# Kernel optimization log

Hardware: AMD Instinct MI355X
Metric: run time of the kernel (lower is better)

The kernel has to match this reference:

```python
import jax, jax.numpy as jnp
import numpy as np

HEADS = 16
GRID_SIZE = 5      # efficient-KAN default
SPLINE_ORDER = 3   # efficient-KAN default


def _grid(in_features, dtype):
    # grid_range = [-1, 1]
    h = 2.0 / GRID_SIZE
    g = jnp.arange(-SPLINE_ORDER, GRID_SIZE + SPLINE_ORDER + 1, dtype=dtype) * h - 1.0
    return jnp.broadcast_to(g, (in_features, g.shape[0]))  # (in, G)


def _b_splines(x, grid):
    # x: (N, in), grid: (in, G); Cox-de Boor recursion
    xg = x[:, :, None]
    bases = ((xg >= grid[:, :-1]) & (xg < grid[:, 1:])).astype(x.dtype)
    for k in range(1, SPLINE_ORDER + 1):
        bases = ((xg - grid[:, :-(k + 1)]) / (grid[:, k:-1] - grid[:, :-(k + 1)]) * bases[:, :, :-1]
                 + (grid[:, k + 1:] - xg) / (grid[:, k + 1:] - grid[:, 1:-k]) * bases[:, :, 1:])
    return bases  # (N, in, GRID_SIZE + SPLINE_ORDER)


def _kan_linear(x, base_w, spline_w, spline_scaler):
    grid = _grid(x.shape[-1], x.dtype)
    base = jax.nn.silu(x) @ base_w.T                      # (N, out)
    b = _b_splines(x, grid)                               # (N, in, K)
    sw = spline_w * spline_scaler[..., None]              # (out, in, K)
    return base + jnp.einsum('nik,oik->no', b, sw)


def setup_inputs():
    key = jax.random.key(0)
    S, H = 2048, 1024
    hd = H // HEADS
    K = GRID_SIZE + SPLINE_ORDER
    ks = jax.random.split(key, 6)
    x = jax.random.normal(ks[0], (S, H), jnp.float32)
    base_w = jax.random.normal(ks[1], (3 * H, H), jnp.float32) / np.float32(np.sqrt(H))
    spline_w = jax.random.normal(ks[2], (3 * H, H, K), jnp.float32) * 0.1
    spline_scaler = 1.0 + 0.1 * jax.random.normal(ks[3], (3 * H, H), jnp.float32)
    out_w = jax.random.normal(ks[4], (H, H), jnp.float32) / np.float32(np.sqrt(H))
    out_b = jnp.zeros((H,), jnp.float32)
    # RoPE rotation matrix (unit complex), theta = 10000
    t = jnp.arange(S, dtype=jnp.float32)
    freqs = 1.0 / (10000.0 ** (jnp.arange(0, hd, 2, dtype=jnp.float32) / hd))
    ang = jnp.outer(t, freqs)  # (S, hd//2)
    return {"x": x, "base_w": base_w, "spline_w": spline_w,
            "spline_scaler": spline_scaler, "out_w": out_w, "out_b": out_b,
            "rot_cos": jnp.cos(ang), "rot_sin": jnp.sin(ang)}


def reference(x, base_w, spline_w, spline_scaler, out_w, out_b, rot_cos, rot_sin):
    S, H = x.shape
    hd = H // HEADS
    qkv = _kan_linear(x, base_w, spline_w, spline_scaler)          # (S, 3H)
    qkv = qkv.reshape(1, S, HEADS, 3 * hd).transpose(0, 2, 1, 3)   # (1,h,S,3d)
    q, k, v = jnp.split(qkv, 3, axis=-1)                           # each (1,h,S,d)

    def rope(t):
        tp = t.reshape(1, HEADS, S, hd // 2, 2)
        c = rot_cos[None, None]
        s = rot_sin[None, None]
        re = tp[..., 0] * c - tp[..., 1] * s
        im = tp[..., 0] * s + tp[..., 1] * c
        return jnp.stack([re, im], axis=-1).reshape(1, HEADS, S, hd)

    q, k = rope(q), rope(k)
    scores = jnp.einsum('bhqd,bhkd->bhqk', q, k) / np.float32(np.sqrt(hd))
    attn = jax.nn.softmax(scores, axis=-1)
    ctx = jnp.einsum('bhqk,bhkd->bhqd', attn, v)
    ctx = ctx.transpose(0, 2, 1, 3).reshape(1, S, H)
    return ctx @ out_w.T + out_b
```

## Files before the change

### kernel.cpp

```cpp
#include <hip/hip_runtime.h>

typedef unsigned short u16;
typedef __bf16 bf16x8 __attribute__((ext_vector_type(8)));
typedef float f32x4 __attribute__((ext_vector_type(4)));

#define S_LEN 2048
#define NHEADS 16
#define HD 64
#define HDIM 1024
#define QKVN 3072
#define KAUG 9216

__device__ __forceinline__ u16 f2bf(float f) {
  union { float f; unsigned u; } v; v.f = f;
  unsigned r = v.u + 0x7fffu + ((v.u >> 16) & 1u);
  return (u16)(r >> 16);
}

typedef __attribute__((address_space(1))) const unsigned int gas_u32;
typedef __attribute__((address_space(3))) unsigned int las_u32;
__device__ __forceinline__ void gload_lds16(const void* g, void* l) {
  __builtin_amdgcn_global_load_lds((gas_u32*)g, (las_u32*)l, 16, 0, 0);
}

__global__ void prep_a_kernel(const float* __restrict__ x, u16* __restrict__ Aaug) {
  int idx = blockIdx.x * 256 + threadIdx.x;
  int n = idx >> 10, i = idx & 1023;
  float xv = x[idx];
  float sil = xv / (1.0f + __expf(-xv));
  Aaug[(size_t)n * KAUG + i] = f2bf(sil);

  float b[11];
#pragma unroll
  for (int j = 0; j < 11; ++j) {
    float t0 = 0.4f * (float)(j - 3) - 1.0f;
    float t1 = 0.4f * (float)(j - 2) - 1.0f;
    b[j] = (xv >= t0 && xv < t1) ? 1.0f : 0.0f;
  }
#pragma unroll
  for (int k = 1; k <= 3; ++k) {
    const float invk = (k == 1) ? 2.5f : (k == 2) ? 1.25f : 0.83333333f;
#pragma unroll
    for (int j = 0; j < 10; ++j) {
      if (j + k < 11) {
        float tj   = 0.4f * (float)(j - 3) - 1.0f;
        float tjk1 = 0.4f * (float)(j + k - 2) - 1.0f;
        b[j] = ((xv - tj) * b[j] + (tjk1 - xv) * b[j + 1]) * invk;
      }
    }
  }
  u16 t[8];
#pragma unroll
  for (int j = 0; j < 8; ++j) t[j] = f2bf(b[j]);
  uint4 pk;
  pk.x = (unsigned)t[0] | ((unsigned)t[1] << 16);
  pk.y = (unsigned)t[2] | ((unsigned)t[3] << 16);
  pk.z = (unsigned)t[4] | ((unsigned)t[5] << 16);
  pk.w = (unsigned)t[6] | ((unsigned)t[7] << 16);
  *reinterpret_cast<uint4*>(&Aaug[(size_t)n * KAUG + 1024 + i * 8]) = pk;
}

__global__ void prep_w_kernel(const float* __restrict__ bw, const float* __restrict__ sw,
                              const float* __restrict__ sc, u16* __restrict__ Waug) {
  int idx = blockIdx.x * 256 + threadIdx.x;
  int o = idx >> 10, i = idx & 1023;
  Waug[(size_t)o * KAUG + i] = f2bf(bw[idx]);
  float s = sc[idx];
  const float4* sp = reinterpret_cast<const float4*>(sw + (size_t)idx * 8);
  float4 a = sp[0], b = sp[1];
  uint4 pk;
  pk.x = (unsigned)f2bf(a.x * s) | ((unsigned)f2bf(a.y * s) << 16);
  pk.y = (unsigned)f2bf(a.z * s) | ((unsigned)f2bf(a.w * s) << 16);
  pk.z = (unsigned)f2bf(b.x * s) | ((unsigned)f2bf(b.y * s) << 16);
  pk.w = (unsigned)f2bf(b.z * s) | ((unsigned)f2bf(b.w * s) << 16);
  *reinterpret_cast<uint4*>(&Waug[(size_t)o * KAUG + 1024 + i * 8]) = pk;
}

__global__ void prep_ow_kernel(const float* __restrict__ ow, u16* __restrict__ owbf) {
  int idx = blockIdx.x * 256 + threadIdx.x;
  float4 v = reinterpret_cast<const float4*>(ow)[idx];
  uint2 pk;
  pk.x = (unsigned)f2bf(v.x) | ((unsigned)f2bf(v.y) << 16);
  pk.y = (unsigned)f2bf(v.z) | ((unsigned)f2bf(v.w) << 16);
  reinterpret_cast<uint2*>(owbf)[idx] = pk;
}

__global__ __launch_bounds__(256) void gemm_bt(
    const u16* __restrict__ A, const u16* __restrict__ B, float* __restrict__ C,
    int M, int N, int K, int Ksp)
{
  __shared__ u16 As[128 * 32];
  __shared__ u16 Bs[128 * 32];
  const int tid = threadIdx.x;
  const int lane = tid & 63;
  const int w = tid >> 6;
  const int wr = w >> 1, wc = w & 1;
  const int row0 = blockIdx.y * 128, col0 = blockIdx.x * 128;
  const int lr = lane & 15, lg = lane >> 4;
  const int kbeg = blockIdx.z * Ksp;
  const int nsteps = Ksp >> 5;
  float* Cz = C + (size_t)blockIdx.z * M * N;

  f32x4 acc[4][4];
#pragma unroll
  for (int m = 0; m < 4; ++m)
#pragma unroll
    for (int n = 0; n < 4; ++n) acc[m][n] = (f32x4){0.f, 0.f, 0.f, 0.f};

  const int arow = tid >> 2;
  const int kch  = tid & 3;
  const u16* ga = A + (size_t)(row0 + arow) * K + kbeg + kch * 8;
  const u16* gb = B + (size_t)(col0 + arow) * K + kbeg + kch * 8;
  const size_t rstep = (size_t)64 * K;

  for (int ks = 0; ks < nsteps; ++ks) {
    gload_lds16(ga, &As[tid * 8]);
    gload_lds16(ga + rstep, &As[2048 + tid * 8]);
    gload_lds16(gb, &Bs[tid * 8]);
    gload_lds16(gb + rstep, &Bs[2048 + tid * 8]);
    ga += 32; gb += 32;
    __syncthreads();

    bf16x8 af[4], bf[4];
#pragma unroll
    for (int m = 0; m < 4; ++m) {
      int r = wr * 64 + m * 16 + lr;
      af[m] = *reinterpret_cast<const bf16x8*>(&As[r * 32 + lg * 8]);
    }
#pragma unroll
    for (int n = 0; n < 4; ++n) {
      int r = wc * 64 + n * 16 + lr;
      bf[n] = *reinterpret_cast<const bf16x8*>(&Bs[r * 32 + lg * 8]);
    }
#pragma unroll
    for (int m = 0; m < 4; ++m)
#pragma unroll
      for (int n = 0; n < 4; ++n)
        acc[m][n] = __builtin_amdgcn_mfma_f32_16x16x32_bf16(af[m], bf[n], acc[m][n], 0, 0, 0);
    __syncthreads();
  }

#pragma unroll
  for (int m = 0; m < 4; ++m) {
    int row = row0 + wr * 64 + m * 16 + lg * 4;
#pragma unroll
    for (int n = 0; n < 4; ++n) {
      int col = col0 + wc * 64 + n * 16 + lr;
#pragma unroll
      for (int j = 0; j < 4; ++j)
        Cz[(size_t)(row + j) * N + col] = acc[m][n][j];
    }
  }
}

__global__ void reduce4_bias_kernel(const float* __restrict__ p, const float* __restrict__ bias,
                                    float* __restrict__ out) {
  int idx = blockIdx.x * 256 + threadIdx.x;
  const float4* p4 = reinterpret_cast<const float4*>(p);
  const size_t stride4 = (size_t)2048 * 1024 / 4;
  float4 a = p4[idx], b = p4[idx + stride4], c = p4[idx + 2 * stride4], d = p4[idx + 3 * stride4];
  float4 bv = reinterpret_cast<const float4*>(bias)[idx & 255];
  float4 r;
  r.x = a.x + b.x + c.x + d.x + bv.x;
  r.y = a.y + b.y + c.y + d.y + bv.y;
  r.z = a.z + b.z + c.z + d.z + bv.z;
  r.w = a.w + b.w + c.w + d.w + bv.w;
  reinterpret_cast<float4*>(out)[idx] = r;
}

__global__ void rope_kernel(const float* __restrict__ qkv0, const float* __restrict__ qkv1,
                            const float* __restrict__ rc, const float* __restrict__ rs,
                            u16* __restrict__ qro, u16* __restrict__ kro) {
  int idx = blockIdx.x * 256 + threadIdx.x;
  int h = idx >> 16;
  int rem = idx & 65535;
  int s = rem >> 5, i = rem & 31;
  size_t boff = (size_t)s * QKVN + h * 192 + 2 * i;
  float2 q0v = *reinterpret_cast<const float2*>(qkv0 + boff);
  float2 q1v = *reinterpret_cast<const float2*>(qkv1 + boff);
  float2 k0v = *reinterpret_cast<const float2*>(qkv0 + boff + 64);
  float2 k1v = *reinterpret_cast<const float2*>(qkv1 + boff + 64);
  float q0 = q0v.x + q1v.x, q1 = q0v.y + q1v.y;
  float k0 = k0v.x + k1v.x, k1 = k0v.y + k1v.y;
  float c = rc[s * 32 + i], sn = rs[s * 32 + i];
  size_t ob = ((size_t)(h * S_LEN + s)) * HD + 2 * i;
  unsigned qpk = (unsigned)f2bf((q0 * c - q1 * sn) * 0.125f) |
                 ((unsigned)f2bf((q0 * sn + q1 * c) * 0.125f) << 16);
  unsigned kpk = (unsigned)f2bf(k0 * c - k1 * sn) |
                 ((unsigned)f2bf(k0 * sn + k1 * c) << 16);
  *reinterpret_cast<unsigned*>(qro + ob) = qpk;
  *reinterpret_cast<unsigned*>(kro + ob) = kpk;
}

__global__ void vtrans_kernel(const float* __restrict__ qkv0, const float* __restrict__ qkv1,
                              u16* __restrict__ vT) {
  __shared__ float tile[64][65];
  int h = blockIdx.x >> 5;
  int st = blockIdx.x & 31;
  int s0 = st * 64;
  int t = threadIdx.x;
  int r = t >> 2, c4 = t & 3;
  size_t soff = (size_t)(s0 + r) * QKVN + h * 192 + 128 + c4 * 16;
  const float* src0 = qkv0 + soff;
  const float* src1 = qkv1 + soff;
#pragma unroll
  for (int z = 0; z < 4; ++z) {
    float4 v = *reinterpret_cast<const float4*>(src0 + z * 4);
    float4 u = *reinterpret_cast<const float4*>(src1 + z * 4);
    tile[r][c4 * 16 + z * 4 + 0] = v.x + u.x;
    tile[r][c4 * 16 + z * 4 + 1] = v.y + u.y;
    tile[r][c4 * 16 + z * 4 + 2] = v.z + u.z;
    tile[r][c4 * 16 + z * 4 + 3] = v.w + u.w;
  }
  __syncthreads();
  int d = t >> 2, sc = t & 3;
  u16* dst = vT + ((size_t)(h * 64 + d)) * S_LEN + s0 + sc * 16;
  unsigned wv[8];
#pragma unroll
  for (int z = 0; z < 8; ++z) {
    unsigned lo = f2bf(tile[sc * 16 + 2 * z][d]);
    unsigned hi = f2bf(tile[sc * 16 + 2 * z + 1][d]);
    wv[z] = lo | (hi << 16);
  }
  *reinterpret_cast<uint4*>(dst)     = make_uint4(wv[0], wv[1], wv[2], wv[3]);
  *reinterpret_cast<uint4*>(dst + 8) = make_uint4(wv[4], wv[5], wv[6], wv[7]);
}

__global__ __launch_bounds__(256) void attn_kernel(
    const u16* __restrict__ qro, const u16* __restrict__ kro,
    const u16* __restrict__ vT, u16* __restrict__ ctxb)
{
  const int lane = threadIdx.x & 63;
  const int w = threadIdx.x >> 6;
  const int bid = (blockIdx.x & 7) * 64 + (blockIdx.x >> 3);
  const int h = bid >> 5;
  const int qt = (bid & 31) * 4 + w;
  const int lr = lane & 15, lg = lane >> 4;

  const u16* qbase = qro + ((size_t)(h * S_LEN + qt * 16 + lr)) * HD + lg * 8;
  bf16x8 qa0 = *reinterpret_cast<const bf16x8*>(qbase);
  bf16x8 qa1 = *reinterpret_cast<const bf16x8*>(qbase + 32);

  float mrow = -3.0e38f, lrow = 0.f;
  f32x4 o[4];
#pragma unroll
  for (int n = 0; n < 4; ++n) o[n] = (f32x4){0.f, 0.f, 0.f, 0.f};

  const int sA = lr + 32 * (lg & 1);
  const int sB = sA + 16;
  const bool loHalf = (lg < 2);

  for (int kt = 0; kt < 64; ++kt) {
    const int key0 = kt * 32;
    const u16* kb = kro + ((size_t)(h * S_LEN + key0 + lr)) * HD + lg * 8;
    bf16x8 k00 = *reinterpret_cast<const bf16x8*>(kb);
    bf16x8 k01 = *reinterpret_cast<const bf16x8*>(kb + 32);
    bf16x8 k10 = *reinterpret_cast<const bf16x8*>(kb + (size_t)16 * HD);
    bf16x8 k11 = *reinterpret_cast<const bf16x8*>(kb + (size_t)16 * HD + 32);

    f32x4 s0 = (f32x4){0.f, 0.f, 0.f, 0.f};
    f32x4 s1 = (f32x4){0.f, 0.f, 0.f, 0.f};
    __builtin_amdgcn_s_setprio(1);
    s0 = __builtin_amdgcn_mfma_f32_16x16x32_bf16(k00, qa0, s0, 0, 0, 0);
    s0 = __builtin_amdgcn_mfma_f32_16x16x32_bf16(k01, qa1, s0, 0, 0, 0);
    s1 = __builtin_amdgcn_mfma_f32_16x16x32_bf16(k10, qa0, s1, 0, 0, 0);
    s1 = __builtin_amdgcn_mfma_f32_16x16x32_bf16(k11, qa1, s1, 0, 0, 0);
    __builtin_amdgcn_s_setprio(0);

    float vmax = fmaxf(fmaxf(fmaxf(s0[0], s0[1]), fmaxf(s0[2], s0[3])),
                       fmaxf(fmaxf(s1[0], s1[1]), fmaxf(s1[2], s1[3])));
    vmax = fmaxf(vmax, __shfl_xor(vmax, 16));
    vmax = fmaxf(vmax, __shfl_xor(vmax, 32));

    if (__any(vmax > mrow + 8.0f)) {
      float mnew = fmaxf(mrow, vmax);
      float al = __expf(mrow - mnew);
      float alO[4];
#pragma unroll
      for (int j = 0; j < 4; ++j) alO[j] = __shfl(al, lg * 4 + j);
#pragma unroll
      for (int n = 0; n < 4; ++n)
#pragma unroll
        for (int j = 0; j < 4; ++j) o[n][j] *= alO[j];
      lrow *= al;
      mrow = mnew;
    }

    float p[8];
#pragma unroll
    for (int j = 0; j < 4; ++j) {
      p[j]     = __expf(s0[j] - mrow);
      p[4 + j] = __expf(s1[j] - mrow);
    }
    lrow += ((p[0] + p[1]) + (p[2] + p[3])) + ((p[4] + p[5]) + (p[6] + p[7]));

    union { bf16x8 v; uint4 u; } pk_;
#pragma unroll
    for (int j = 0; j < 8; ++j) pk_.v[j] = (__bf16)p[j];

    unsigned a0 = __shfl((int)pk_.u.x, sA), a1 = __shfl((int)pk_.u.y, sA);
    unsigned a2 = __shfl((int)pk_.u.x, sB), a3 = __shfl((int)pk_.u.y, sB);
    unsigned b0 = __shfl((int)pk_.u.z, sA), b1 = __shfl((int)pk_.u.w, sA);
    unsigned b2 = __shfl((int)pk_.u.z, sB), b3 = __shfl((int)pk_.u.w, sB);
    union { uint4 u; bf16x8 v; } pa_;
    pa_.u.x = loHalf ? a0 : b0;
    pa_.u.y = loHalf ? a1 : b1;
    pa_.u.z = loHalf ? a2 : b2;
    pa_.u.w = loHalf ? a3 : b3;

    const u16* vb = vT + ((size_t)(h * 64 + lr)) * S_LEN + key0 + lg * 8;
    __builtin_amdgcn_s_setprio(1);
#pragma unroll
    for (int n = 0; n < 4; ++n) {
      bf16x8 vf = *reinterpret_cast<const bf16x8*>(vb + (size_t)(n * 16) * S_LEN);
      o[n] = __builtin_amdgcn_mfma_f32_16x16x32_bf16(pa_.v, vf, o[n], 0, 0, 0);
    }
    __builtin_amdgcn_s_setprio(0);
  }

  lrow += __shfl_xor(lrow, 16);
  lrow += __shfl_xor(lrow, 32);
  float linv[4];
#pragma unroll
  for (int j = 0; j < 4; ++j) linv[j] = 1.0f / __shfl(lrow, lg * 4 + j);

#pragma unroll
  for (int n = 0; n < 4; ++n) {
    int col = h * 64 + n * 16 + lr;
#pragma unroll
    for (int j = 0; j < 4; ++j) {
      int row = qt * 16 + lg * 4 + j;
      ctxb[(size_t)row * HDIM + col] = f2bf(o[n][j] * linv[j]);
    }
  }
}

extern "C" void kernel_launch(void* const* d_in, const int* in_sizes, int n_in,
                              void* d_out, int out_size, void* d_ws, size_t ws_size,
                              hipStream_t stream) {
  const float* x   = (const float*)d_in[0];
  const float* bw  = (const float*)d_in[1];
  const float* sw  = (const float*)d_in[2];
  const float* ssc = (const float*)d_in[3];
  const float* ow  = (const float*)d_in[4];
  const float* ob  = (const float*)d_in[5];
  const float* rc  = (const float*)d_in[6];
  const float* rs  = (const float*)d_in[7];
  float* out = (float*)d_out;

  char* ws = (char*)d_ws;
  u16*   Aaug  = (u16*)(ws);
  u16*   Waug  = (u16*)(ws + 37748736);
  float* qkv0  = (float*)(ws + 94371840);
  float* qkv1  = (float*)(ws + 119537664);
  u16*   qro   = (u16*)(ws + 144703488);
  u16*   kro   = (u16*)(ws + 148897792);
  u16*   vT    = (u16*)(ws + 153092096);
  u16*   owbf  = (u16*)(ws + 157286400);
  u16*   ctxb  = (u16*)(ws + 94371840);
  float* part  = (float*)(ws + 119537664);

  prep_a_kernel<<<8192, 256, 0, stream>>>(x, Aaug);
  prep_w_kernel<<<12288, 256, 0, stream>>>(bw, sw, ssc, Waug);
  prep_ow_kernel<<<1024, 256, 0, stream>>>(ow, owbf);

  gemm_bt<<<dim3(24, 16, 2), 256, 0, stream>>>(Aaug, Waug, qkv0, 2048, 3072, 9216, 4608);

  rope_kernel<<<4096, 256, 0, stream>>>(qkv0, qkv1, rc, rs, qro, kro);
  vtrans_kernel<<<512, 256, 0, stream>>>(qkv0, qkv1, vT);

  attn_kernel<<<512, 256, 0, stream>>>(qro, kro, vT, ctxb);

  gemm_bt<<<dim3(8, 16, 4), 256, 0, stream>>>(ctxb, owbf, part, 2048, 1024, 1024, 256);
  reduce4_bias_kernel<<<2048, 256, 0, stream>>>(part, ob, out);
}
```

Before: 499.5 us.

## Raise QKV GEMM split-K to four and prefetch K/V tiles in attention

The QKV GEMM split-K factor becomes four when the workspace is large enough, giving 768 blocks instead of 384 for better CU occupancy. The rope and vtrans kernels are generalised to sum a variable number of partial buffers. The attention loop now loads the next K tile one iteration ahead and issues the V loads early to hide memory latency. The cost is extra partial-buffer traffic and more registers in attention.

```diff
diff --git a/kernel.cpp b/kernel.cpp
--- a/kernel.cpp
+++ b/kernel.cpp
@@ -168,7 +168,7 @@
   reinterpret_cast<float4*>(out)[idx] = r;
 }
 
-__global__ void rope_kernel(const float* __restrict__ qkv0, const float* __restrict__ qkv1,
+__global__ void rope_kernel(const float* __restrict__ qkv, int nsplit,
                             const float* __restrict__ rc, const float* __restrict__ rs,
                             u16* __restrict__ qro, u16* __restrict__ kro) {
   int idx = blockIdx.x * 256 + threadIdx.x;
@@ -176,12 +176,14 @@
   int rem = idx & 65535;
   int s = rem >> 5, i = rem & 31;
   size_t boff = (size_t)s * QKVN + h * 192 + 2 * i;
-  float2 q0v = *reinterpret_cast<const float2*>(qkv0 + boff);
-  float2 q1v = *reinterpret_cast<const float2*>(qkv1 + boff);
-  float2 k0v = *reinterpret_cast<const float2*>(qkv0 + boff + 64);
-  float2 k1v = *reinterpret_cast<const float2*>(qkv1 + boff + 64);
-  float q0 = q0v.x + q1v.x, q1 = q0v.y + q1v.y;
-  float k0 = k0v.x + k1v.x, k1 = k0v.y + k1v.y;
+  const size_t zstr = (size_t)S_LEN * QKVN;
+  float q0 = 0.f, q1 = 0.f, k0 = 0.f, k1 = 0.f;
+  for (int z = 0; z < nsplit; ++z) {
+    const float* b = qkv + z * zstr + boff;
+    float2 qv = *reinterpret_cast<const float2*>(b);
+    float2 kv = *reinterpret_cast<const float2*>(b + 64);
+    q0 += qv.x; q1 += qv.y; k0 += kv.x; k1 += kv.y;
+  }
   float c = rc[s * 32 + i], sn = rs[s * 32 + i];
   size_t ob = ((size_t)(h * S_LEN + s)) * HD + 2 * i;
   unsigned qpk = (unsigned)f2bf((q0 * c - q1 * sn) * 0.125f) |
@@ -192,7 +194,7 @@
   *reinterpret_cast<unsigned*>(kro + ob) = kpk;
 }
 
-__global__ void vtrans_kernel(const float* __restrict__ qkv0, const float* __restrict__ qkv1,
+__global__ void vtrans_kernel(const float* __restrict__ qkv, int nsplit,
                               u16* __restrict__ vT) {
   __shared__ float tile[64][65];
   int h = blockIdx.x >> 5;
@@ -201,16 +203,18 @@
   int t = threadIdx.x;
   int r = t >> 2, c4 = t & 3;
   size_t soff = (size_t)(s0 + r) * QKVN + h * 192 + 128 + c4 * 16;
-  const float* src0 = qkv0 + soff;
-  const float* src1 = qkv1 + soff;
-#pragma unroll
-  for (int z = 0; z < 4; ++z) {
-    float4 v = *reinterpret_cast<const float4*>(src0 + z * 4);
-    float4 u = *reinterpret_cast<const float4*>(src1 + z * 4);
-    tile[r][c4 * 16 + z * 4 + 0] = v.x + u.x;
-    tile[r][c4 * 16 + z * 4 + 1] = v.y + u.y;
-    tile[r][c4 * 16 + z * 4 + 2] = v.z + u.z;
-    tile[r][c4 * 16 + z * 4 + 3] = v.w + u.w;
+  const size_t zstr = (size_t)S_LEN * QKVN;
+#pragma unroll
+  for (int z4 = 0; z4 < 4; ++z4) {
+    float acc4[4] = {0.f, 0.f, 0.f, 0.f};
+    for (int z = 0; z < nsplit; ++z) {
+      float4 v = *reinterpret_cast<const float4*>(qkv + z * zstr + soff + z4 * 4);
+      acc4[0] += v.x; acc4[1] += v.y; acc4[2] += v.z; acc4[3] += v.w;
+    }
+    tile[r][c4 * 16 + z4 * 4 + 0] = acc4[0];
+    tile[r][c4 * 16 + z4 * 4 + 1] = acc4[1];
+    tile[r][c4 * 16 + z4 * 4 + 2] = acc4[2];
+    tile[r][c4 * 16 + z4 * 4 + 3] = acc4[3];
   }
   __syncthreads();
   int d = t >> 2, sc = t & 3;
@@ -250,21 +254,33 @@
   const int sB = sA + 16;
   const bool loHalf = (lg < 2);
 
+  const u16* kbase = kro + ((size_t)(h * S_LEN + lr)) * HD + lg * 8;
+  const u16* vbase = vT + ((size_t)(h * 64 + lr)) * S_LEN + lg * 8;
+
+  bf16x8 kc00 = *reinterpret_cast<const bf16x8*>(kbase);
+  bf16x8 kc01 = *reinterpret_cast<const bf16x8*>(kbase + 32);
+  bf16x8 kc10 = *reinterpret_cast<const bf16x8*>(kbase + 16 * HD);
+  bf16x8 kc11 = *reinterpret_cast<const bf16x8*>(kbase + 16 * HD + 32);
+
   for (int kt = 0; kt < 64; ++kt) {
-    const int key0 = kt * 32;
-    const u16* kb = kro + ((size_t)(h * S_LEN + key0 + lr)) * HD + lg * 8;
-    bf16x8 k00 = *reinterpret_cast<const bf16x8*>(kb);
-    bf16x8 k01 = *reinterpret_cast<const bf16x8*>(kb + 32);
-    bf16x8 k10 = *reinterpret_cast<const bf16x8*>(kb + (size_t)16 * HD);
-    bf16x8 k11 = *reinterpret_cast<const bf16x8*>(kb + (size_t)16 * HD + 32);
+    const u16* vb = vbase + kt * 32;
+    bf16x8 vf0 = *reinterpret_cast<const bf16x8*>(vb);
+    bf16x8 vf1 = *reinterpret_cast<const bf16x8*>(vb + (size_t)16 * S_LEN);
+    bf16x8 vf2 = *reinterpret_cast<const bf16x8*>(vb + (size_t)32 * S_LEN);
+    bf16x8 vf3 = *reinterpret_cast<const bf16x8*>(vb + (size_t)48 * S_LEN);
+    const u16* knb = kbase + (size_t)(((kt + 1) & 63) * 32) * HD;
+    bf16x8 kn00 = *reinterpret_cast<const bf16x8*>(knb);
+    bf16x8 kn01 = *reinterpret_cast<const bf16x8*>(knb + 32);
+    bf16x8 kn10 = *reinterpret_cast<const bf16x8*>(knb + 16 * HD);
+    bf16x8 kn11 = *reinterpret_cast<const bf16x8*>(knb + 16 * HD + 32);
 
     f32x4 s0 = (f32x4){0.f, 0.f, 0.f, 0.f};
     f32x4 s1 = (f32x4){0.f, 0.f, 0.f, 0.f};
     __builtin_amdgcn_s_setprio(1);
-    s0 = __builtin_amdgcn_mfma_f32_16x16x32_bf16(k00, qa0, s0, 0, 0, 0);
-    s0 = __builtin_amdgcn_mfma_f32_16x16x32_bf16(k01, qa1, s0, 0, 0, 0);
-    s1 = __builtin_amdgcn_mfma_f32_16x16x32_bf16(k10, qa0, s1, 0, 0, 0);
-    s1 = __builtin_amdgcn_mfma_f32_16x16x32_bf16(k11, qa1, s1, 0, 0, 0);
+    s0 = __builtin_amdgcn_mfma_f32_16x16x32_bf16(kc00, qa0, s0, 0, 0, 0);
+    s0 = __builtin_amdgcn_mfma_f32_16x16x32_bf16(kc01, qa1, s0, 0, 0, 0);
+    s1 = __builtin_amdgcn_mfma_f32_16x16x32_bf16(kc10, qa0, s1, 0, 0, 0);
+    s1 = __builtin_amdgcn_mfma_f32_16x16x32_bf16(kc11, qa1, s1, 0, 0, 0);
     __builtin_amdgcn_s_setprio(0);
 
     float vmax = fmaxf(fmaxf(fmaxf(s0[0], s0[1]), fmaxf(s0[2], s0[3])),
@@ -308,14 +324,14 @@
     pa_.u.z = loHalf ? a2 : b2;
     pa_.u.w = loHalf ? a3 : b3;
 
-    const u16* vb = vT + ((size_t)(h * 64 + lr)) * S_LEN + key0 + lg * 8;
     __builtin_amdgcn_s_setprio(1);
-#pragma unroll
-    for (int n = 0; n < 4; ++n) {
-      bf16x8 vf = *reinterpret_cast<const bf16x8*>(vb + (size_t)(n * 16) * S_LEN);
-      o[n] = __builtin_amdgcn_mfma_f32_16x16x32_bf16(pa_.v, vf, o[n], 0, 0, 0);
-    }
+    o[0] = __builtin_amdgcn_mfma_f32_16x16x32_bf16(pa_.v, vf0, o[0], 0, 0, 0);
+    o[1] = __builtin_amdgcn_mfma_f32_16x16x32_bf16(pa_.v, vf1, o[1], 0, 0, 0);
+    o[2] = __builtin_amdgcn_mfma_f32_16x16x32_bf16(pa_.v, vf2, o[2], 0, 0, 0);
+    o[3] = __builtin_amdgcn_mfma_f32_16x16x32_bf16(pa_.v, vf3, o[3], 0, 0, 0);
     __builtin_amdgcn_s_setprio(0);
+
+    kc00 = kn00; kc01 = kn01; kc10 = kn10; kc11 = kn11;
   }
 
   lrow += __shfl_xor(lrow, 16);
@@ -349,25 +365,29 @@
   float* out = (float*)d_out;
 
   char* ws = (char*)d_ws;
+  const size_t MNF = 25165824;
+  const int splitk = (ws_size >= (size_t)209715200) ? 4 : 2;
+
   u16*   Aaug  = (u16*)(ws);
   u16*   Waug  = (u16*)(ws + 37748736);
-  float* qkv0  = (float*)(ws + 94371840);
-  float* qkv1  = (float*)(ws + 119537664);
-  u16*   qro   = (u16*)(ws + 144703488);
-  u16*   kro   = (u16*)(ws + 148897792);
-  u16*   vT    = (u16*)(ws + 153092096);
-  u16*   owbf  = (u16*)(ws + 157286400);
+  float* qkv   = (float*)(ws + 94371840);
+  size_t qend  = 94371840 + (size_t)splitk * MNF;
+  u16*   qro   = (u16*)(ws + qend);
+  u16*   kro   = (u16*)(ws + qend + 4194304);
+  u16*   vT    = (u16*)(ws + qend + 8388608);
+  u16*   owbf  = (u16*)(ws + qend + 12582912);
   u16*   ctxb  = (u16*)(ws + 94371840);
-  float* part  = (float*)(ws + 119537664);
+  float* part  = (float*)(ws + 94371840 + MNF);
 
   prep_a_kernel<<<8192, 256, 0, stream>>>(x, Aaug);
   prep_w_kernel<<<12288, 256, 0, stream>>>(bw, sw, ssc, Waug);
   prep_ow_kernel<<<1024, 256, 0, stream>>>(ow, owbf);
 
-  gemm_bt<<<dim3(24, 16, 2), 256, 0, stream>>>(Aaug, Waug, qkv0, 2048, 3072, 9216, 4608);
-
-  rope_kernel<<<4096, 256, 0, stream>>>(qkv0, qkv1, rc, rs, qro, kro);
-  vtrans_kernel<<<512, 256, 0, stream>>>(qkv0, qkv1, vT);
+  gemm_bt<<<dim3(24, 16, splitk), 256, 0, stream>>>(Aaug, Waug, qkv, 2048, 3072, 9216,
+                                                    9216 / splitk);
+
+  rope_kernel<<<4096, 256, 0, stream>>>(qkv, splitk, rc, rs, qro, kro);
+  vtrans_kernel<<<512, 256, 0, stream>>>(qkv, splitk, vT);
 
   attn_kernel<<<512, 256, 0, stream>>>(qro, kro, vT, ctxb);
 
```

Measured after the change: 523.8 us. 4.9% more time.
